# Kernel tuning notes

Measured on AMD Instinct MI355X. Metric: run time of the kernel, lower is better.

The kernel has to match this reference:

```python
import jax, jax.numpy as jnp
import numpy as np

B, N, D_IN, D_OUT, R = 8, 1024, 256, 256, 4


def setup_inputs() -> dict:
    key = jax.random.key(0)
    ks = jax.random.split(key, 8)
    scale_in = 1.0 / np.sqrt(D_IN)
    scale_out = 1.0 / np.sqrt(2 * D_OUT)
    scale_g = 1.0 / np.sqrt(D_OUT)
    return {
        "node_features": jax.random.normal(ks[0], (B, N, D_IN), dtype=jnp.float32),
        "adj_matrix": jax.random.randint(ks[1], (B, R, N, N), 0, 2, dtype=jnp.int32),
        "rel_w": jax.random.uniform(ks[2], (R, D_OUT, D_IN), jnp.float32, -scale_in, scale_in),
        "rel_b": jax.random.uniform(ks[3], (R, D_OUT), jnp.float32, -scale_in, scale_in),
        "attn_w": jax.random.uniform(ks[4], (2 * D_OUT,), jnp.float32, -scale_out, scale_out),
        "attn_b": jax.random.uniform(ks[5], (), jnp.float32, -scale_out, scale_out),
        "gate_w": jax.random.uniform(ks[6], (D_OUT,), jnp.float32, -scale_g, scale_g),
        "gate_b": jax.random.uniform(ks[7], (), jnp.float32, -scale_g, scale_g),
    }


def reference(node_features, adj_matrix, rel_w, rel_b, attn_w, attn_b, gate_w, gate_b):
    # Per-relation projections: [B, R, N, D]
    feats = jnp.einsum('bni,rdi->brnd', node_features, rel_w) + rel_b[None, :, None, :]
    # attn_proj(cat([h_i, h_j])) == h_i @ w_i + h_j @ w_j + b  (linear over concat)
    d = feats.shape[-1]
    si = jnp.einsum('brnd,d->brn', feats, attn_w[:d])   # contribution of row node i
    sj = jnp.einsum('brnd,d->brn', feats, attn_w[d:])   # contribution of col node j
    score = si[:, :, :, None] + sj[:, :, None, :] + attn_b  # [B, R, N, N]
    score = jnp.where(adj_matrix == 0, jnp.float32(-1e9), score)
    attn = jax.nn.softmax(score, axis=-1)
    # Aggregate over relations: sum_r attn_r @ feats_r -> [B, N, D]
    agg = jnp.einsum('brnm,brmd->bnd', attn, feats)
    gate = jax.nn.sigmoid(jnp.einsum('bnd,d->bn', agg, gate_w) + gate_b)
    return gate[:, :, None] * agg
```

## Files before the change

### kernel.cpp

```cpp
#include <hip/hip_runtime.h>
#include <hip/hip_bf16.h>

#define B_ 8
#define N_ 1024
#define DIN 256
#define DOUT 256
#define R_ 4

typedef __attribute__((ext_vector_type(8))) short bf16x8;
typedef __attribute__((ext_vector_type(4))) float f32x4;
typedef __attribute__((ext_vector_type(4))) int i32x4;

__device__ __forceinline__ unsigned short f2bf(float f) {
    union { float f; unsigned int u; } v; v.f = f;
    unsigned int u = v.u;
    u += 0x7fffu + ((u >> 16) & 1u);
    return (unsigned short)(u >> 16);
}
__device__ __forceinline__ float bf2f(unsigned short h) {
    union { float f; unsigned int u; } v; v.u = ((unsigned int)h) << 16;
    return v.f;
}

__device__ __forceinline__ void gl_lds16(const void* g, void* l) {
    __builtin_amdgcn_global_load_lds(
        (const __attribute__((address_space(1))) unsigned int*)g,
        (__attribute__((address_space(3))) unsigned int*)l, 16, 0, 0);
}

__global__ __launch_bounds__(256) void k0_swz(const float* __restrict__ rw,
                                              unsigned short* __restrict__ swzW) {
    int t = blockIdx.x * 256 + threadIdx.x;
    int lane = t & 63, nb = (t >> 6) & 15, ks = (t >> 10) & 7, r = t >> 13;
    int m = lane & 15, q = lane >> 4;
    const float* src = rw + ((r * DOUT + nb * 16 + m) * DIN) + ks * 32 + q * 8;
    float4 v0 = *(const float4*)src;
    float4 v1 = *(const float4*)(src + 4);
    bf16x8 o;
    o[0] = (short)f2bf(v0.x); o[1] = (short)f2bf(v0.y);
    o[2] = (short)f2bf(v0.z); o[3] = (short)f2bf(v0.w);
    o[4] = (short)f2bf(v1.x); o[5] = (short)f2bf(v1.y);
    o[6] = (short)f2bf(v1.z); o[7] = (short)f2bf(v1.w);
    *(bf16x8*)(swzW + (long)t * 8) = o;
}

__global__ __launch_bounds__(256) void k1_proj(const float* __restrict__ node,
        const unsigned short* __restrict__ swzW, const float* __restrict__ rel_b,
        const float* __restrict__ attn_w,
        unsigned short* __restrict__ fswz, unsigned short* __restrict__ ebf) {
    __shared__ unsigned short Wbuf[2][8192];
    int bid = blockIdx.x;
    int nt = bid & 15, r = (bid >> 4) & 3, b = bid >> 6;
    int w = threadIdx.x >> 6, lane = threadIdx.x & 63;
    int m = lane & 15, q = lane >> 4;
    int n0 = nt * 64 + w * 16;

    const float* Abase = node + ((b * N_ + n0 + m) * DIN) + q * 8;
    const unsigned short* Wsrc = swzW + r * 65536;

#pragma unroll
    for (int i = 0; i < 4; i++)
        gl_lds16(Wsrc + (w * 4 + i) * 512 + lane * 8, &Wbuf[0][(w * 4 + i) * 512]);

    f32x4 acc[16];
#pragma unroll
    for (int i = 0; i < 16; i++) acc[i] = (f32x4)0.0f;

    float4 a0 = *(const float4*)(Abase);
    float4 a1 = *(const float4*)(Abase + 4);

    for (int ks = 0; ks < 8; ks++) {
        int cur = ks & 1;
        __syncthreads();
        if (ks < 7) {
#pragma unroll
            for (int i = 0; i < 4; i++)
                gl_lds16(Wsrc + ((ks + 1) * 16 + w * 4 + i) * 512 + lane * 8,
                         &Wbuf[cur ^ 1][(w * 4 + i) * 512]);
        }
        bf16x8 af;
        af[0] = (short)f2bf(a0.x); af[1] = (short)f2bf(a0.y);
        af[2] = (short)f2bf(a0.z); af[3] = (short)f2bf(a0.w);
        af[4] = (short)f2bf(a1.x); af[5] = (short)f2bf(a1.y);
        af[6] = (short)f2bf(a1.z); af[7] = (short)f2bf(a1.w);
        if (ks < 7) {
            a0 = *(const float4*)(Abase + (ks + 1) * 32);
            a1 = *(const float4*)(Abase + (ks + 1) * 32 + 4);
        }
#pragma unroll
        for (int nb = 0; nb < 16; nb++) {
            bf16x8 wf = *(const bf16x8*)(&Wbuf[cur][nb * 512 + lane * 8]);
            acc[nb] = __builtin_amdgcn_mfma_f32_16x16x32_bf16(af, wf, acc[nb], 0, 0, 0);
        }
    }

    float sj0 = 0.f, sj1 = 0.f, sj2 = 0.f, sj3 = 0.f;
    float bias[16], aw[16];
#pragma unroll
    for (int nb = 0; nb < 16; nb++) {
        int d = nb * 16 + m;
        bias[nb] = rel_b[r * DOUT + d];
        aw[nb] = attn_w[DOUT + d];
        sj0 += (acc[nb][0] + bias[nb]) * aw[nb];
        sj1 += (acc[nb][1] + bias[nb]) * aw[nb];
        sj2 += (acc[nb][2] + bias[nb]) * aw[nb];
        sj3 += (acc[nb][3] + bias[nb]) * aw[nb];
    }
#pragma unroll
    for (int mk = 1; mk <= 8; mk <<= 1) {
        sj0 += __shfl_xor(sj0, mk, 64);
        sj1 += __shfl_xor(sj1, mk, 64);
        sj2 += __shfl_xor(sj2, mk, 64);
        sj3 += __shfl_xor(sj3, mk, 64);
    }
    float e0 = __expf(sj0), e1 = __expf(sj1), e2 = __expf(sj2), e3 = __expf(sj3);

    int slice = b * R_ + r;
    int js = n0 >> 5;
    int jhi = (n0 >> 4) & 1;
    int qp = jhi * 2 + (q >> 1);
    int jj0 = (q & 1) * 4;
    unsigned short* fb = fswz + ((long)(slice * 32 + js) * 16) * 512
                       + qp * 128 + m * 8 + jj0;
#pragma unroll
    for (int nb = 0; nb < 16; nb++) {
        ushort4 o;
        o.x = f2bf((acc[nb][0] + bias[nb]) * e0);
        o.y = f2bf((acc[nb][1] + bias[nb]) * e1);
        o.z = f2bf((acc[nb][2] + bias[nb]) * e2);
        o.w = f2bf((acc[nb][3] + bias[nb]) * e3);
        *(ushort4*)(fb + nb * 512) = o;
    }
    if (m == 0) {
        ushort4 o;
        o.x = f2bf(e0); o.y = f2bf(e1); o.z = f2bf(e2); o.w = f2bf(e3);
        *(ushort4*)(ebf + slice * N_ + n0 + q * 4) = o;
    }
}

__global__ __launch_bounds__(256) void k2_pack(const int* __restrict__ adj,
                                               unsigned int* __restrict__ pk) {
    int t = blockIdx.x * 256 + threadIdx.x;
    const int* src = adj + (size_t)t * 32;
    i32x4 v[8];
#pragma unroll
    for (int i = 0; i < 8; i++) v[i] = *(const i32x4*)(src + i * 4);
    unsigned int bits = 0;
#pragma unroll
    for (int i = 0; i < 8; i++) {
        bits |= (v[i].x ? 1u : 0u) << (4 * i);
        bits |= (v[i].y ? 2u : 0u) << (4 * i);
        bits |= (v[i].z ? 4u : 0u) << (4 * i);
        bits |= (v[i].w ? 8u : 0u) << (4 * i);
    }
    pk[t] = bits;
}

__global__ __launch_bounds__(256, 2) void k3_attn(const unsigned int* __restrict__ pk,
        const unsigned short* __restrict__ fswz, const unsigned short* __restrict__ ebf,
        unsigned short* __restrict__ aggU, float* __restrict__ lbuf) {
    __shared__ unsigned short Gbuf[2][8192];
    __shared__ unsigned short Ebuf[512];

    int bid = blockIdx.x;
    int slice = (bid & 7) * 4 + ((bid >> 3) & 3);
    int rest = bid >> 5;
    int pair = rest & 7, jh = rest >> 3;
    int t = threadIdx.x, lane = t & 63, w = t >> 6;
    int m = lane & 15, q = lane >> 4;
    int i0b = pair * 128;

    const unsigned short* fsl = fswz + ((size_t)(slice * 32 + jh * 16)) * 8192;
    const unsigned short* esl = ebf + slice * N_ + jh * 512;

    const unsigned int* pA = pk + ((size_t)slice * N_ + i0b + w * 16 + m) * 32 + jh * 16;
    const unsigned int* pB = pA + 64 * 32;
    unsigned int Wa[16], Wb[16];
#pragma unroll
    for (int i = 0; i < 4; i++) *(i32x4*)(&Wa[i * 4]) = *(const i32x4*)(pA + i * 4);
#pragma unroll
    for (int i = 0; i < 4; i++) *(i32x4*)(&Wb[i * 4]) = *(const i32x4*)(pB + i * 4);
    int q8 = q * 8;

#pragma unroll
    for (int i = 0; i < 4; i++)
        gl_lds16(fsl + (w * 4 + i) * 512 + lane * 8, &Gbuf[0][(w * 4 + i) * 512]);
    if (w == 0)
        gl_lds16(esl + lane * 8, &Ebuf[0]);

    f32x4 accA[16], accB[16];
#pragma unroll
    for (int i = 0; i < 16; i++) { accA[i] = (f32x4)0.0f; accB[i] = (f32x4)0.0f; }
    float lA = 0.f, lB = 0.f;

#pragma unroll
    for (int s = 0; s < 16; s++) {
        int cur = s & 1;
        __syncthreads();
        if (s < 15) {
#pragma unroll
            for (int i = 0; i < 4; i++)
                gl_lds16(fsl + (size_t)(s + 1) * 8192 + (w * 4 + i) * 512 + lane * 8,
                         &Gbuf[cur ^ 1][(w * 4 + i) * 512]);
        }
        unsigned int byteA = (Wa[s] >> q8) & 0xffu;
        unsigned int byteB = (Wb[s] >> q8) & 0xffu;
        bf16x8 ev = *(const bf16x8*)(&Ebuf[s * 32 + q * 8]);
        const int* ei = (const int*)&ev;
        bf16x8 afA, afB;
        int* aiA = (int*)&afA;
        int* aiB = (int*)&afB;
#pragma unroll
        for (int p = 0; p < 4; p++) {
            unsigned int mA = (((byteA >> (2 * p)) & 1u) ? 0xffffu : 0u)
                            | (((byteA >> (2 * p + 1)) & 1u) ? 0xffff0000u : 0u);
            unsigned int mB = (((byteB >> (2 * p)) & 1u) ? 0xffffu : 0u)
                            | (((byteB >> (2 * p + 1)) & 1u) ? 0xffff0000u : 0u);
            aiA[p] = (int)(mA & 0x3F803F80u);
            aiB[p] = (int)(mB & 0x3F803F80u);
            int meA = ei[p] & (int)mA;
            int meB = ei[p] & (int)mB;
            union { int i; float f; } lo, hi;
            lo.i = meA << 16; hi.i = meA & (int)0xffff0000u;
            lA += lo.f + hi.f;
            lo.i = meB << 16; hi.i = meB & (int)0xffff0000u;
            lB += lo.f + hi.f;
        }
        const unsigned short* Gb = &Gbuf[cur][lane * 8];
#pragma unroll
        for (int nb = 0; nb < 16; nb++) {
            bf16x8 bfq = *(const bf16x8*)(Gb + nb * 512);
            accA[nb] = __builtin_amdgcn_mfma_f32_16x16x32_bf16(afA, bfq, accA[nb], 0, 0, 0);
            accB[nb] = __builtin_amdgcn_mfma_f32_16x16x32_bf16(afB, bfq, accB[nb], 0, 0, 0);
        }
    }

    lA += __shfl_xor(lA, 16, 64);
    lA += __shfl_xor(lA, 32, 64);
    lB += __shfl_xor(lB, 16, 64);
    lB += __shfl_xor(lB, 32, 64);
    int half = slice * 2 + jh;
    if (lane < 16) {
        lbuf[half * N_ + i0b + w * 16 + lane] = lA;
        lbuf[half * N_ + i0b + 64 + w * 16 + lane] = lB;
    }

    unsigned short* obA = aggU + ((size_t)half * N_ + i0b + w * 16 + q * 4) * DOUT + m;
    unsigned short* obB = obA + (size_t)64 * DOUT;
#pragma unroll
    for (int nb = 0; nb < 16; nb++) {
#pragma unroll
        for (int reg = 0; reg < 4; reg++) {
            obA[(size_t)reg * DOUT + nb * 16] = f2bf(accA[nb][reg]);
            obB[(size_t)reg * DOUT + nb * 16] = f2bf(accB[nb][reg]);
        }
    }
}

__global__ __launch_bounds__(256) void k4_out(const unsigned short* __restrict__ aggU,
        const float* __restrict__ lbuf, const float* __restrict__ gate_w,
        const float* __restrict__ gate_b, float* __restrict__ out) {
    __shared__ float red[4];
    int bid = blockIdx.x;
    int n = bid & 1023, b = bid >> 10;
    int d = threadIdx.x;
    float s = 0.f;
#pragma unroll
    for (int r = 0; r < R_; r++) {
        int sl = b * R_ + r;
        float a0 = bf2f(aggU[((size_t)(sl * 2 + 0) * N_ + n) * DOUT + d]);
        float a1 = bf2f(aggU[((size_t)(sl * 2 + 1) * N_ + n) * DOUT + d]);
        float lt = lbuf[(sl * 2 + 0) * N_ + n] + lbuf[(sl * 2 + 1) * N_ + n];
        float inv = (lt > 0.f) ? 1.0f / lt : 0.f;
        s += (a0 + a1) * inv;
    }
    float v = s * gate_w[d];
#pragma unroll
    for (int off = 32; off; off >>= 1) v += __shfl_down(v, off, 64);
    int lane = d & 63, wave = d >> 6;
    if (lane == 0) red[wave] = v;
    __syncthreads();
    float tot = red[0] + red[1] + red[2] + red[3];
    float g = 1.f / (1.f + __expf(-(tot + gate_b[0])));
    out[((long)(b * N_ + n)) * DOUT + d] = g * s;
}

extern "C" void kernel_launch(void* const* d_in, const int* in_sizes, int n_in,
                              void* d_out, int out_size, void* d_ws, size_t ws_size,
                              hipStream_t stream) {
    const float* node   = (const float*)d_in[0];
    const int*   adj    = (const int*)d_in[1];
    const float* rel_w  = (const float*)d_in[2];
    const float* rel_b  = (const float*)d_in[3];
    const float* attn_w = (const float*)d_in[4];
    const float* gate_w = (const float*)d_in[6];
    const float* gate_b = (const float*)d_in[7];
    float* out = (float*)d_out;

    char* ws = (char*)d_ws;
    unsigned short* swzW = (unsigned short*)ws;
    unsigned short* fswz = (unsigned short*)(ws + 524288);
    unsigned short* ebf  = (unsigned short*)(ws + 17301504);
    unsigned short* aggU = (unsigned short*)(ws + 17367040);
    float*          lbuf = (float*)(ws + 50921472);
    unsigned int*   pk   = (unsigned int*)(ws + 51183616);

    k0_swz<<<128, 256, 0, stream>>>(rel_w, swzW);
    k2_pack<<<4096, 256, 0, stream>>>(adj, pk);
    k1_proj<<<512, 256, 0, stream>>>(node, swzW, rel_b, attn_w, fswz, ebf);
    k3_attn<<<512, 256, 0, stream>>>(pk, fswz, ebf, aggU, lbuf);
    k4_out<<<8192, 256, 0, stream>>>(aggU, lbuf, gate_w, gate_b, out);
}
```

Baseline: 256.8 us.

## Give each projection wave two row tiles and vectorise output kernel per wave

The projection kernel now runs 128 threads (2 waves) per block, and each wave computes two 16-row tiles that share every LDS weight fragment. This halves LDS weight reads per MFMA but doubles the accumulator registers per thread. The output kernel now handles one node per wave with 4-wide vector loads and stores, and reduces with shuffles only, removing the shared-memory reduction and block barrier. Fewer waves per block may reduce latency hiding in the projection kernel.

```diff
diff --git a/kernel.cpp b/kernel.cpp
--- a/kernel.cpp
+++ b/kernel.cpp
@@ -44,7 +44,7 @@
     *(bf16x8*)(swzW + (long)t * 8) = o;
 }
 
-__global__ __launch_bounds__(256) void k1_proj(const float* __restrict__ node,
+__global__ __launch_bounds__(128, 2) void k1_proj(const float* __restrict__ node,
         const unsigned short* __restrict__ swzW, const float* __restrict__ rel_b,
         const float* __restrict__ attn_w,
         unsigned short* __restrict__ fswz, unsigned short* __restrict__ ebf) {
@@ -53,88 +53,110 @@
     int nt = bid & 15, r = (bid >> 4) & 3, b = bid >> 6;
     int w = threadIdx.x >> 6, lane = threadIdx.x & 63;
     int m = lane & 15, q = lane >> 4;
-    int n0 = nt * 64 + w * 16;
-
-    const float* Abase = node + ((b * N_ + n0 + m) * DIN) + q * 8;
+    int n0 = nt * 64 + w * 32;
+
+    const float* AbaseA = node + ((b * N_ + n0 + m) * DIN) + q * 8;
+    const float* AbaseB = AbaseA + 16 * DIN;
     const unsigned short* Wsrc = swzW + r * 65536;
 
 #pragma unroll
-    for (int i = 0; i < 4; i++)
-        gl_lds16(Wsrc + (w * 4 + i) * 512 + lane * 8, &Wbuf[0][(w * 4 + i) * 512]);
-
-    f32x4 acc[16];
-#pragma unroll
-    for (int i = 0; i < 16; i++) acc[i] = (f32x4)0.0f;
-
-    float4 a0 = *(const float4*)(Abase);
-    float4 a1 = *(const float4*)(Abase + 4);
+    for (int i = 0; i < 8; i++)
+        gl_lds16(Wsrc + (w * 8 + i) * 512 + lane * 8, &Wbuf[0][(w * 8 + i) * 512]);
+
+    f32x4 accA[16], accB[16];
+#pragma unroll
+    for (int i = 0; i < 16; i++) { accA[i] = (f32x4)0.0f; accB[i] = (f32x4)0.0f; }
+
+    float4 a0A = *(const float4*)(AbaseA);
+    float4 a1A = *(const float4*)(AbaseA + 4);
+    float4 a0B = *(const float4*)(AbaseB);
+    float4 a1B = *(const float4*)(AbaseB + 4);
 
     for (int ks = 0; ks < 8; ks++) {
         int cur = ks & 1;
         __syncthreads();
         if (ks < 7) {
 #pragma unroll
-            for (int i = 0; i < 4; i++)
-                gl_lds16(Wsrc + ((ks + 1) * 16 + w * 4 + i) * 512 + lane * 8,
-                         &Wbuf[cur ^ 1][(w * 4 + i) * 512]);
-        }
-        bf16x8 af;
-        af[0] = (short)f2bf(a0.x); af[1] = (short)f2bf(a0.y);
-        af[2] = (short)f2bf(a0.z); af[3] = (short)f2bf(a0.w);
-        af[4] = (short)f2bf(a1.x); af[5] = (short)f2bf(a1.y);
-        af[6] = (short)f2bf(a1.z); af[7] = (short)f2bf(a1.w);
+            for (int i = 0; i < 8; i++)
+                gl_lds16(Wsrc + ((ks + 1) * 16 + w * 8 + i) * 512 + lane * 8,
+                         &Wbuf[cur ^ 1][(w * 8 + i) * 512]);
+        }
+        bf16x8 afA, afB;
+        afA[0] = (short)f2bf(a0A.x); afA[1] = (short)f2bf(a0A.y);
+        afA[2] = (short)f2bf(a0A.z); afA[3] = (short)f2bf(a0A.w);
+        afA[4] = (short)f2bf(a1A.x); afA[5] = (short)f2bf(a1A.y);
+        afA[6] = (short)f2bf(a1A.z); afA[7] = (short)f2bf(a1A.w);
+        afB[0] = (short)f2bf(a0B.x); afB[1] = (short)f2bf(a0B.y);
+        afB[2] = (short)f2bf(a0B.z); afB[3] = (short)f2bf(a0B.w);
+        afB[4] = (short)f2bf(a1B.x); afB[5] = (short)f2bf(a1B.y);
+        afB[6] = (short)f2bf(a1B.z); afB[7] = (short)f2bf(a1B.w);
         if (ks < 7) {
-            a0 = *(const float4*)(Abase + (ks + 1) * 32);
-            a1 = *(const float4*)(Abase + (ks + 1) * 32 + 4);
+            a0A = *(const float4*)(AbaseA + (ks + 1) * 32);
+            a1A = *(const float4*)(AbaseA + (ks + 1) * 32 + 4);
+            a0B = *(const float4*)(AbaseB + (ks + 1) * 32);
+            a1B = *(const float4*)(AbaseB + (ks + 1) * 32 + 4);
         }
 #pragma unroll
         for (int nb = 0; nb < 16; nb++) {
             bf16x8 wf = *(const bf16x8*)(&Wbuf[cur][nb * 512 + lane * 8]);
-            acc[nb] = __builtin_amdgcn_mfma_f32_16x16x32_bf16(af, wf, acc[nb], 0, 0, 0);
-        }
-    }
-
-    float sj0 = 0.f, sj1 = 0.f, sj2 = 0.f, sj3 = 0.f;
+            accA[nb] = __builtin_amdgcn_mfma_f32_16x16x32_bf16(afA, wf, accA[nb], 0, 0, 0);
+            accB[nb] = __builtin_amdgcn_mfma_f32_16x16x32_bf16(afB, wf, accB[nb], 0, 0, 0);
+        }
+    }
+
+    float sA0 = 0.f, sA1 = 0.f, sA2 = 0.f, sA3 = 0.f;
+    float sB0 = 0.f, sB1 = 0.f, sB2 = 0.f, sB3 = 0.f;
     float bias[16], aw[16];
 #pragma unroll
     for (int nb = 0; nb < 16; nb++) {
         int d = nb * 16 + m;
         bias[nb] = rel_b[r * DOUT + d];
         aw[nb] = attn_w[DOUT + d];
-        sj0 += (acc[nb][0] + bias[nb]) * aw[nb];
-        sj1 += (acc[nb][1] + bias[nb]) * aw[nb];
-        sj2 += (acc[nb][2] + bias[nb]) * aw[nb];
-        sj3 += (acc[nb][3] + bias[nb]) * aw[nb];
+        sA0 += (accA[nb][0] + bias[nb]) * aw[nb];
+        sA1 += (accA[nb][1] + bias[nb]) * aw[nb];
+        sA2 += (accA[nb][2] + bias[nb]) * aw[nb];
+        sA3 += (accA[nb][3] + bias[nb]) * aw[nb];
+        sB0 += (accB[nb][0] + bias[nb]) * aw[nb];
+        sB1 += (accB[nb][1] + bias[nb]) * aw[nb];
+        sB2 += (accB[nb][2] + bias[nb]) * aw[nb];
+        sB3 += (accB[nb][3] + bias[nb]) * aw[nb];
     }
 #pragma unroll
     for (int mk = 1; mk <= 8; mk <<= 1) {
-        sj0 += __shfl_xor(sj0, mk, 64);
-        sj1 += __shfl_xor(sj1, mk, 64);
-        sj2 += __shfl_xor(sj2, mk, 64);
-        sj3 += __shfl_xor(sj3, mk, 64);
-    }
-    float e0 = __expf(sj0), e1 = __expf(sj1), e2 = __expf(sj2), e3 = __expf(sj3);
+        sA0 += __shfl_xor(sA0, mk, 64); sA1 += __shfl_xor(sA1, mk, 64);
+        sA2 += __shfl_xor(sA2, mk, 64); sA3 += __shfl_xor(sA3, mk, 64);
+        sB0 += __shfl_xor(sB0, mk, 64); sB1 += __shfl_xor(sB1, mk, 64);
+        sB2 += __shfl_xor(sB2, mk, 64); sB3 += __shfl_xor(sB3, mk, 64);
+    }
+    float eA0 = __expf(sA0), eA1 = __expf(sA1), eA2 = __expf(sA2), eA3 = __expf(sA3);
+    float eB0 = __expf(sB0), eB1 = __expf(sB1), eB2 = __expf(sB2), eB3 = __expf(sB3);
 
     int slice = b * R_ + r;
     int js = n0 >> 5;
-    int jhi = (n0 >> 4) & 1;
-    int qp = jhi * 2 + (q >> 1);
     int jj0 = (q & 1) * 4;
-    unsigned short* fb = fswz + ((long)(slice * 32 + js) * 16) * 512
-                       + qp * 128 + m * 8 + jj0;
+    unsigned short* base = fswz + ((long)(slice * 32 + js) * 16) * 512 + m * 8 + jj0;
+    unsigned short* fbA = base + (0 * 2 + (q >> 1)) * 128;
+    unsigned short* fbB = base + (1 * 2 + (q >> 1)) * 128;
 #pragma unroll
     for (int nb = 0; nb < 16; nb++) {
-        ushort4 o;
-        o.x = f2bf((acc[nb][0] + bias[nb]) * e0);
-        o.y = f2bf((acc[nb][1] + bias[nb]) * e1);
-        o.z = f2bf((acc[nb][2] + bias[nb]) * e2);
-        o.w = f2bf((acc[nb][3] + bias[nb]) * e3);
-        *(ushort4*)(fb + nb * 512) = o;
+        ushort4 oA, oB;
+        oA.x = f2bf((accA[nb][0] + bias[nb]) * eA0);
+        oA.y = f2bf((accA[nb][1] + bias[nb]) * eA1);
+        oA.z = f2bf((accA[nb][2] + bias[nb]) * eA2);
+        oA.w = f2bf((accA[nb][3] + bias[nb]) * eA3);
+        oB.x = f2bf((accB[nb][0] + bias[nb]) * eB0);
+        oB.y = f2bf((accB[nb][1] + bias[nb]) * eB1);
+        oB.z = f2bf((accB[nb][2] + bias[nb]) * eB2);
+        oB.w = f2bf((accB[nb][3] + bias[nb]) * eB3);
+        *(ushort4*)(fbA + nb * 512) = oA;
+        *(ushort4*)(fbB + nb * 512) = oB;
     }
     if (m == 0) {
-        ushort4 o;
-        o.x = f2bf(e0); o.y = f2bf(e1); o.z = f2bf(e2); o.w = f2bf(e3);
-        *(ushort4*)(ebf + slice * N_ + n0 + q * 4) = o;
+        ushort4 oA, oB;
+        oA.x = f2bf(eA0); oA.y = f2bf(eA1); oA.z = f2bf(eA2); oA.w = f2bf(eA3);
+        oB.x = f2bf(eB0); oB.y = f2bf(eB1); oB.z = f2bf(eB2); oB.w = f2bf(eB3);
+        *(ushort4*)(ebf + slice * N_ + n0 + q * 4) = oA;
+        *(ushort4*)(ebf + slice * N_ + n0 + 16 + q * 4) = oB;
     }
 }
 
@@ -260,29 +282,32 @@
 __global__ __launch_bounds__(256) void k4_out(const unsigned short* __restrict__ aggU,
         const float* __restrict__ lbuf, const float* __restrict__ gate_w,
         const float* __restrict__ gate_b, float* __restrict__ out) {
-    __shared__ float red[4];
-    int bid = blockIdx.x;
-    int n = bid & 1023, b = bid >> 10;
-    int d = threadIdx.x;
-    float s = 0.f;
+    int w = threadIdx.x >> 6, lane = threadIdx.x & 63;
+    int n = blockIdx.x * 4 + w;
+    int nn = n & 1023, b = n >> 10;
+    int d0 = lane * 4;
+    float s0 = 0.f, s1 = 0.f, s2 = 0.f, s3 = 0.f;
 #pragma unroll
     for (int r = 0; r < R_; r++) {
         int sl = b * R_ + r;
-        float a0 = bf2f(aggU[((size_t)(sl * 2 + 0) * N_ + n) * DOUT + d]);
-        float a1 = bf2f(aggU[((size_t)(sl * 2 + 1) * N_ + n) * DOUT + d]);
-        float lt = lbuf[(sl * 2 + 0) * N_ + n] + lbuf[(sl * 2 + 1) * N_ + n];
+        ushort4 u0 = *(const ushort4*)(aggU + ((size_t)(sl * 2 + 0) * N_ + nn) * DOUT + d0);
+        ushort4 u1 = *(const ushort4*)(aggU + ((size_t)(sl * 2 + 1) * N_ + nn) * DOUT + d0);
+        float lt = lbuf[(sl * 2 + 0) * N_ + nn] + lbuf[(sl * 2 + 1) * N_ + nn];
         float inv = (lt > 0.f) ? 1.0f / lt : 0.f;
-        s += (a0 + a1) * inv;
-    }
-    float v = s * gate_w[d];
+        s0 += (bf2f(u0.x) + bf2f(u1.x)) * inv;
+        s1 += (bf2f(u0.y) + bf2f(u1.y)) * inv;
+        s2 += (bf2f(u0.z) + bf2f(u1.z)) * inv;
+        s3 += (bf2f(u0.w) + bf2f(u1.w)) * inv;
+    }
+    float4 gw = *(const float4*)(gate_w + d0);
+    float v = s0 * gw.x + s1 * gw.y + s2 * gw.z + s3 * gw.w;
 #pragma unroll
     for (int off = 32; off; off >>= 1) v += __shfl_down(v, off, 64);
-    int lane = d & 63, wave = d >> 6;
-    if (lane == 0) red[wave] = v;
-    __syncthreads();
-    float tot = red[0] + red[1] + red[2] + red[3];
+    float tot = __shfl(v, 0, 64);
     float g = 1.f / (1.f + __expf(-(tot + gate_b[0])));
-    out[((long)(b * N_ + n)) * DOUT + d] = g * s;
+    float4 o;
+    o.x = g * s0; o.y = g * s1; o.z = g * s2; o.w = g * s3;
+    *(float4*)(out + ((long)(b * N_ + nn)) * DOUT + d0) = o;
 }
 
 extern "C" void kernel_launch(void* const* d_in, const int* in_sizes, int n_in,
@@ -307,7 +332,7 @@
 
     k0_swz<<<128, 256, 0, stream>>>(rel_w, swzW);
     k2_pack<<<4096, 256, 0, stream>>>(adj, pk);
-    k1_proj<<<512, 256, 0, stream>>>(node, swzW, rel_b, attn_w, fswz, ebf);
+    k1_proj<<<512, 128, 0, stream>>>(node, swzW, rel_b, attn_w, fswz, ebf);
     k3_attn<<<512, 256, 0, stream>>>(pk, fswz, ebf, aggU, lbuf);
-    k4_out<<<8192, 256, 0, stream>>>(aggU, lbuf, gate_w, gate_b, out);
-}
+    k4_out<<<2048, 256, 0, stream>>>(aggU, lbuf, gate_w, gate_b, out);
+}
```

Result: no change. 256.3 us (-0.2%).
